# Kernel optimization log

Measured on AMD Instinct MI355X. Metric: run time of the kernel, lower is better.

The kernel has to match this reference:

```python
import jax, jax.numpy as jnp
import numpy as np

S, B, C = 7, 2, 20
D = C + 5 * B  # 30
LAMBDA_COORD = 5.0
LAMBDA_NOOBJ = 0.5
EPS = 1e-6


def _iou_yolo(b1, b2):
    # b1, b2: [..., 4] boxes in (cx, cy, w, h) 'yolo' format
    b1x1 = b1[..., 0] - b1[..., 2] / 2
    b1y1 = b1[..., 1] - b1[..., 3] / 2
    b1x2 = b1[..., 0] + b1[..., 2] / 2
    b1y2 = b1[..., 1] + b1[..., 3] / 2
    b2x1 = b2[..., 0] - b2[..., 2] / 2
    b2y1 = b2[..., 1] - b2[..., 3] / 2
    b2x2 = b2[..., 0] + b2[..., 2] / 2
    b2y2 = b2[..., 1] + b2[..., 3] / 2
    iw = jnp.clip(jnp.minimum(b1x2, b2x2) - jnp.maximum(b1x1, b2x1), 0.0)
    ih = jnp.clip(jnp.minimum(b1y2, b2y2) - jnp.maximum(b1y1, b2y1), 0.0)
    inter = iw * ih
    a1 = jnp.abs((b1x2 - b1x1) * (b1y2 - b1y1))
    a2 = jnp.abs((b2x2 - b2x1) * (b2y2 - b2y1))
    return inter / (a1 + a2 - inter + EPS)


def setup_inputs() -> dict:
    batch = 16384
    key = jax.random.key(0)
    k1, k2, k3 = jax.random.split(key, 3)
    # true coords / classes in (0.05, 0.95) so sqrt(w), sqrt(h) are well-defined
    y_trues = jax.random.uniform(k1, (batch, S, S, D), dtype=jnp.float32) * 0.9 + 0.05
    conf = (jax.random.uniform(k2, (batch, S, S)) < 0.3).astype(jnp.float32)
    y_trues = y_trues.at[..., 4].set(conf)  # objectness indicator is exactly 0 or 1
    y_preds = jax.random.normal(k3, (batch, S, S, D), dtype=jnp.float32)
    return {"y_trues": y_trues, "y_preds": y_preds}


def reference(y_trues, y_preds):
    yt = y_trues.reshape(-1, S * S, D)
    yp = y_preds.reshape(-1, S * S, D)
    batch = yt.shape[0]

    obj = (yt[..., 4] == 1.0).astype(yt.dtype)   # [N, S*S]
    noobj = 1.0 - obj

    iou1 = _iou_yolo(yt[..., 0:4], yp[..., 0:4])
    iou2 = _iou_yolo(yt[..., 0:4], yp[..., 5:9])
    best1 = iou1 > iou2                           # responsible box selection

    box_hat = jnp.where(best1[..., None], yp[..., 0:4], yp[..., 5:9])
    conf_hat = jnp.where(best1, yp[..., 4], yp[..., 9])        # responsible conf
    other_conf_hat = jnp.where(best1, yp[..., 9], yp[..., 4])  # non-responsible conf

    # xy offset loss
    xy = (yt[..., 0] - box_hat[..., 0]) ** 2 + (yt[..., 1] - box_hat[..., 1]) ** 2
    # wh loss: sqrt(true) vs sqrt(|pred + eps|)
    wh = (jnp.sqrt(yt[..., 2]) - jnp.sqrt(jnp.abs(box_hat[..., 2] + EPS))) ** 2 \
       + (jnp.sqrt(yt[..., 3]) - jnp.sqrt(jnp.abs(box_hat[..., 3] + EPS))) ** 2
    # object confidence loss (true conf == 1 in obj cells)
    obj_conf = (yt[..., 4] - conf_hat) ** 2
    # no-object penalty on the NON-responsible box inside object cells (target 0)
    noobj_in_obj = LAMBDA_NOOBJ * other_conf_hat ** 2
    # no-object penalty on BOTH boxes in cells without objects (true conf == 0)
    noobj_cells = LAMBDA_NOOBJ * ((yt[..., 4] - yp[..., 4]) ** 2
                                  + (yt[..., 4] - yp[..., 9]) ** 2)
    # class loss over C classes
    cls = jnp.sum((yt[..., 10:] - yp[..., 10:]) ** 2, axis=-1)

    per_cell = obj * (LAMBDA_COORD * (xy + wh) + obj_conf + noobj_in_obj + cls) \
             + noobj * noobj_cells
    return jnp.sum(per_cell) / batch
```

## Files before the change

kernel.cpp:

```cpp
#include <hip/hip_runtime.h>


#define SS 49
#define DD 30
#define BLOCK 256
#define WPB 4
#define CPW 64
#define FPW (CPW * DD)
#define F2PW (FPW / 2)
#define PERSIST_GRID 512

__device__ __forceinline__ float iou_yolo(const float b1[4], const float b2[4]) {
    const float EPS = 1e-6f;
    float b1x1 = b1[0] - b1[2] * 0.5f, b1y1 = b1[1] - b1[3] * 0.5f;
    float b1x2 = b1[0] + b1[2] * 0.5f, b1y2 = b1[1] + b1[3] * 0.5f;
    float b2x1 = b2[0] - b2[2] * 0.5f, b2y1 = b2[1] - b2[3] * 0.5f;
    float b2x2 = b2[0] + b2[2] * 0.5f, b2y2 = b2[1] + b2[3] * 0.5f;
    float iw = fmaxf(fminf(b1x2, b2x2) - fmaxf(b1x1, b2x1), 0.0f);
    float ih = fmaxf(fminf(b1y2, b2y2) - fmaxf(b1y1, b2y1), 0.0f);
    float inter = iw * ih;
    float a1 = fabsf((b1x2 - b1x1) * (b1y2 - b1y1));
    float a2 = fabsf((b2x2 - b2x1) * (b2y2 - b2y1));
    return inter / (a1 + a2 - inter + EPS);
}

__device__ __forceinline__ float cell_loss(const float* __restrict__ yt,
                                           const float* __restrict__ yp) {
    const float LAMBDA_COORD = 5.0f;
    const float LAMBDA_NOOBJ = 0.5f;
    const float EPS = 1e-6f;

    float obj = (yt[4] == 1.0f) ? 1.0f : 0.0f;
    float noobj = 1.0f - obj;

    float tb[4]  = {yt[0], yt[1], yt[2], yt[3]};
    float pb1[4] = {yp[0], yp[1], yp[2], yp[3]};
    float pb2[4] = {yp[5], yp[6], yp[7], yp[8]};
    float iou1 = iou_yolo(tb, pb1);
    float iou2 = iou_yolo(tb, pb2);
    bool best1 = iou1 > iou2;

    float bh0 = best1 ? yp[0] : yp[5];
    float bh1 = best1 ? yp[1] : yp[6];
    float bh2 = best1 ? yp[2] : yp[7];
    float bh3 = best1 ? yp[3] : yp[8];
    float conf_hat       = best1 ? yp[4] : yp[9];
    float other_conf_hat = best1 ? yp[9] : yp[4];

    float dx = yt[0] - bh0, dy = yt[1] - bh1;
    float xy = dx * dx + dy * dy;

    float sw = sqrtf(yt[2]) - sqrtf(fabsf(bh2 + EPS));
    float sh = sqrtf(yt[3]) - sqrtf(fabsf(bh3 + EPS));
    float wh = sw * sw + sh * sh;

    float dc = yt[4] - conf_hat;
    float obj_conf = dc * dc;

    float noobj_in_obj = LAMBDA_NOOBJ * other_conf_hat * other_conf_hat;

    float d4 = yt[4] - yp[4];
    float d9 = yt[4] - yp[9];
    float noobj_cells = LAMBDA_NOOBJ * (d4 * d4 + d9 * d9);

    float cls = 0.0f;
#pragma unroll
    for (int k = 10; k < DD; ++k) {
        float d = yt[k] - yp[k];
        cls += d * d;
    }

    return obj * (LAMBDA_COORD * (xy + wh) + obj_conf + noobj_in_obj + cls)
         + noobj * noobj_cells;
}

template <int USE_WS>
__global__ __launch_bounds__(BLOCK)
void yolo_loss_kernel(const float* __restrict__ yt_g,
                      const float* __restrict__ yp_g,
                      float* __restrict__ sink,
                      int ncells, float inv_batch) {
    __shared__ __align__(16) float lt[WPB][FPW];
    __shared__ __align__(16) float lp[WPB][FPW];
    __shared__ float smem[WPB];

    const int tid  = threadIdx.x;
    const int lane = tid & 63;
    const int wave = tid >> 6;
    const int gwave  = blockIdx.x * WPB + wave;
    const int nwaves = gridDim.x * WPB;
    const int nwt = (ncells + CPW - 1) / CPW;

    float* __restrict__ ltw = lt[wave];
    float* __restrict__ lpw = lp[wave];
    float2* __restrict__ ltw2 = reinterpret_cast<float2*>(ltw);
    float2* __restrict__ lpw2 = reinterpret_cast<float2*>(lpw);

    float wsum = 0.0f;

    for (int wt = gwave; wt < nwt; wt += nwaves) {
        const int cb = wt * CPW;
        const size_t f2b = (size_t)cb * (DD / 2);
        const float2* gt2 = reinterpret_cast<const float2*>(yt_g) + f2b;
        const float2* gp2 = reinterpret_cast<const float2*>(yp_g) + f2b;
        const int ncf2 = min(CPW, ncells - cb) * (DD / 2);

        if (ncf2 == F2PW) {
#pragma unroll
            for (int i = 0; i < F2PW / 64; ++i) {
                int idx = i * 64 + lane;
                float2 a = gt2[idx];
                float2 b = gp2[idx];
                ltw2[idx] = a;
                lpw2[idx] = b;
            }
        } else {
#pragma unroll
            for (int i = 0; i < F2PW / 64; ++i) {
                int idx = i * 64 + lane;
                if (idx < ncf2) {
                    ltw2[idx] = gt2[idx];
                    lpw2[idx] = gp2[idx];
                }
            }
        }

        int c = cb + lane;
        if (c < ncells)
            wsum += cell_loss(&ltw[lane * DD], &lpw[lane * DD]);
    }

#pragma unroll
    for (int off = 32; off > 0; off >>= 1)
        wsum += __shfl_down(wsum, off, 64);

    if (lane == 0) smem[wave] = wsum;
    __syncthreads();
    if (tid == 0) {
        float s = smem[0] + smem[1] + smem[2] + smem[3];
        if (USE_WS) sink[blockIdx.x] = s;
        else        atomicAdd(sink, s * inv_batch);
    }
}

__global__ __launch_bounds__(256)
void reduce_kernel(const float* __restrict__ partials, float* __restrict__ out,
                   int n, float inv_batch) {
    float s = 0.0f;
    for (int i = threadIdx.x; i < n; i += 256) s += partials[i];
#pragma unroll
    for (int off = 32; off > 0; off >>= 1)
        s += __shfl_down(s, off, 64);
    __shared__ float sm[4];
    int lane = threadIdx.x & 63;
    int wave = threadIdx.x >> 6;
    if (lane == 0) sm[wave] = s;
    __syncthreads();
    if (threadIdx.x == 0)
        out[0] = (sm[0] + sm[1] + sm[2] + sm[3]) * inv_batch;
}

extern "C" void kernel_launch(void* const* d_in, const int* in_sizes, int n_in,
                              void* d_out, int out_size, void* d_ws, size_t ws_size,
                              hipStream_t stream) {
    const float* yt = (const float*)d_in[0];
    const float* yp = (const float*)d_in[1];
    float* out = (float*)d_out;
    float* ws = (float*)d_ws;

    int total = in_sizes[0];
    int ncells = total / DD;
    int batch = ncells / SS;
    float inv_batch = 1.0f / (float)batch;

    int nwt = (ncells + CPW - 1) / CPW;
    int grid_needed = (nwt + WPB - 1) / WPB;
    int grid = grid_needed < PERSIST_GRID ? grid_needed : PERSIST_GRID;

    if (ws != nullptr && ws_size >= (size_t)grid * sizeof(float)) {
        yolo_loss_kernel<1><<<grid, BLOCK, 0, stream>>>(yt, yp, ws, ncells,
                                                        inv_batch);
        reduce_kernel<<<1, 256, 0, stream>>>(ws, out, grid, inv_batch);
    } else {
        hipMemsetAsync(out, 0, sizeof(float), stream);
        yolo_loss_kernel<0><<<grid, BLOCK, 0, stream>>>(yt, yp, out, ncells,
                                                        inv_batch);
    }
}
```

Before: 206.7 us.

## Register-prefetch next tile with 16-byte nontemporal loads into shared staging

Each wave now loads its next 64-cell tile into registers as float4 nontemporal loads while it computes the current tile from shared memory. The two inputs go into one combined per-wave buffer, and the partial tail tile is handled separately with direct global reads. The intent is to hide global-memory latency behind compute and to issue wider loads. In exchange, register pressure rises (15 float4 per lane), which may lower occupancy, and the LDS write of the next tile is not separated from the current reads by any barrier.

Result: faster. 186.6 us (-9.7%).

```diff
diff --git a/kernel.cpp b/kernel.cpp
--- a/kernel.cpp
+++ b/kernel.cpp
@@ -7,8 +7,12 @@
 #define WPB 4
 #define CPW 64
 #define FPW (CPW * DD)
-#define F2PW (FPW / 2)
+#define F4PT (2 * FPW / 4)
+#define F4PL (F4PT / 64)
+#define HALF_F4 (FPW / 4)
 #define PERSIST_GRID 512
+
+typedef float f32x4 __attribute__((ext_vector_type(4)));
 
 __device__ __forceinline__ float iou_yolo(const float b1[4], const float b2[4]) {
     const float EPS = 1e-6f;
@@ -74,14 +78,35 @@
          + noobj * noobj_cells;
 }
 
+__device__ __forceinline__ void load_tile_nt(f32x4 r[F4PL],
+                                             const f32x4* __restrict__ gt4,
+                                             const f32x4* __restrict__ gp4,
+                                             int lane) {
+#pragma unroll
+    for (int i = 0; i < F4PL; ++i) {
+        int idx = i * 64 + lane;
+        const f32x4* src = (idx < HALF_F4) ? (gt4 + idx)
+                                           : (gp4 + (idx - HALF_F4));
+        r[i] = __builtin_nontemporal_load(src);
+    }
+    __builtin_amdgcn_sched_barrier(0);
+}
+
+__device__ __forceinline__ void write_tile(const f32x4 r[F4PL],
+                                           f32x4* __restrict__ l4, int lane) {
+#pragma unroll
+    for (int i = 0; i < F4PL; ++i)
+        l4[i * 64 + lane] = r[i];
+    __builtin_amdgcn_sched_barrier(0);
+}
+
 template <int USE_WS>
 __global__ __launch_bounds__(BLOCK)
 void yolo_loss_kernel(const float* __restrict__ yt_g,
                       const float* __restrict__ yp_g,
                       float* __restrict__ sink,
                       int ncells, float inv_batch) {
-    __shared__ __align__(16) float lt[WPB][FPW];
-    __shared__ __align__(16) float lp[WPB][FPW];
+    __shared__ __align__(16) float lbuf[WPB][2 * FPW];
     __shared__ float smem[WPB];
 
     const int tid  = threadIdx.x;
@@ -89,45 +114,42 @@
     const int wave = tid >> 6;
     const int gwave  = blockIdx.x * WPB + wave;
     const int nwaves = gridDim.x * WPB;
-    const int nwt = (ncells + CPW - 1) / CPW;
-
-    float* __restrict__ ltw = lt[wave];
-    float* __restrict__ lpw = lp[wave];
-    float2* __restrict__ ltw2 = reinterpret_cast<float2*>(ltw);
-    float2* __restrict__ lpw2 = reinterpret_cast<float2*>(lpw);
+
+    const int nwt_full   = ncells / CPW;
+    const int tail_cells = ncells - nwt_full * CPW;
+
+    float* __restrict__ wb  = lbuf[wave];
+    f32x4* __restrict__ wb4 = reinterpret_cast<f32x4*>(wb);
 
     float wsum = 0.0f;
-
-    for (int wt = gwave; wt < nwt; wt += nwaves) {
-        const int cb = wt * CPW;
-        const size_t f2b = (size_t)cb * (DD / 2);
-        const float2* gt2 = reinterpret_cast<const float2*>(yt_g) + f2b;
-        const float2* gp2 = reinterpret_cast<const float2*>(yp_g) + f2b;
-        const int ncf2 = min(CPW, ncells - cb) * (DD / 2);
-
-        if (ncf2 == F2PW) {
-#pragma unroll
-            for (int i = 0; i < F2PW / 64; ++i) {
-                int idx = i * 64 + lane;
-                float2 a = gt2[idx];
-                float2 b = gp2[idx];
-                ltw2[idx] = a;
-                lpw2[idx] = b;
-            }
-        } else {
-#pragma unroll
-            for (int i = 0; i < F2PW / 64; ++i) {
-                int idx = i * 64 + lane;
-                if (idx < ncf2) {
-                    ltw2[idx] = gt2[idx];
-                    lpw2[idx] = gp2[idx];
-                }
-            }
+    f32x4 r[F4PL];
+
+    int wt = gwave;
+    if (wt < nwt_full) {
+        const size_t fb = (size_t)wt * FPW;
+        load_tile_nt(r, reinterpret_cast<const f32x4*>(yt_g + fb),
+                        reinterpret_cast<const f32x4*>(yp_g + fb), lane);
+    }
+    while (wt < nwt_full) {
+        const int next = wt + nwaves;
+
+        write_tile(r, wb4, lane);
+
+        if (next < nwt_full) {
+            const size_t fb = (size_t)next * FPW;
+            load_tile_nt(r, reinterpret_cast<const f32x4*>(yt_g + fb),
+                            reinterpret_cast<const f32x4*>(yp_g + fb), lane);
         }
 
-        int c = cb + lane;
+        wsum += cell_loss(&wb[lane * DD], &wb[FPW + lane * DD]);
+
+        wt = next;
+    }
+
+    if (tail_cells != 0 && gwave == (nwt_full % nwaves)) {
+        int c = nwt_full * CPW + lane;
         if (c < ncells)
-            wsum += cell_loss(&ltw[lane * DD], &lpw[lane * DD]);
+            wsum += cell_loss(yt_g + (size_t)c * DD, yp_g + (size_t)c * DD);
     }
 
 #pragma unroll
@@ -182,7 +204,7 @@
                                                         inv_batch);
         reduce_kernel<<<1, 256, 0, stream>>>(ws, out, grid, inv_batch);
     } else {
-        hipMemsetAsync(out, 0, sizeof(float), stream);
+        (void)hipMemsetAsync(out, 0, sizeof(float), stream);
         yolo_loss_kernel<0><<<grid, BLOCK, 0, stream>>>(yt, yp, out, ncells,
                                                         inv_batch);
     }
```
